# Kernel optimization log

Measured on AMD Instinct MI355X. Metric: run time of the kernel, lower is better.

The kernel has to match this reference:

```python
import jax, jax.numpy as jnp
from jax import lax
import numpy as np

B, DIM, L_IN = 8, 512, 4096
SCALE = 2
KSIZE = 17
DN = ('NCH', 'OIH', 'NCH')  # conv1d dimension numbers


def _aa_kernel(kernel_size: int, scale: int) -> np.ndarray:
    # replicates scipy.signal.kaiser_atten / kaiser_beta / windows.kaiser
    atten = 2.285 * (kernel_size - 1) * np.pi * (1.0 / scale) + 7.95
    if atten > 50:
        beta = 0.1102 * (atten - 8.7)
    elif atten > 21:
        beta = 0.5842 * (atten - 21) ** 0.4 + 0.07886 * (atten - 21)
    else:
        beta = 0.0
    win = np.kaiser(kernel_size, beta)
    xk = np.arange(kernel_size) - kernel_size // 2
    k = np.sinc(xk / scale) * win  # normalized sinc, same as torch.sinc
    return (k / k.sum()).astype(np.float32)


def setup_inputs() -> dict:
    key = jax.random.key(0)
    k1, k2, k3, k4, k5 = jax.random.split(key, 5)
    kconv = 2 * SCALE - 1
    return {
        'x': jax.random.normal(k1, (B, DIM, L_IN), dtype=jnp.float32),
        'conv_w': jax.random.normal(k2, (DIM, DIM, kconv), dtype=jnp.float32) * (1.0 / np.sqrt(DIM * kconv)),
        'conv_b': jax.random.normal(k3, (DIM,), dtype=jnp.float32) * 0.01,
        'aa_kernel': jnp.asarray(_aa_kernel(KSIZE, SCALE)),
        'proj_w': jax.random.normal(k4, (DIM, DIM), dtype=jnp.float32) * (1.0 / np.sqrt(DIM)),
        'proj_b': jax.random.normal(k5, (DIM,), dtype=jnp.float32) * 0.01,
    }


def reference(x, conv_w, conv_b, aa_kernel, proj_w, proj_b):
    s = SCALE
    # zero-insertion upsample + Conv1d(dim,dim,2s-1,pad=s-1) fused via lhs_dilation.
    # Torch zero-inserts to length l*s (trailing s-1 zeros), so right pad is 2s-2.
    y = lax.conv_general_dilated(
        x, conv_w, window_strides=(1,), padding=[(s - 1, 2 * s - 2)],
        lhs_dilation=(s,), dimension_numbers=DN,
    ) + conv_b[None, :, None]  # [B, D, l*s]
    # depthwise anti-alias filter (same Kaiser-sinc kernel per channel)
    dw = jnp.broadcast_to(aa_kernel, (DIM, 1, KSIZE))
    y = lax.conv_general_dilated(
        y, dw, window_strides=(1,), padding=[(KSIZE // 2, KSIZE // 2)],
        feature_group_count=DIM, dimension_numbers=DN,
    )
    # pointwise 1x1 projection
    return jnp.einsum('bdl,ed->bel', y, proj_w) + proj_b[None, :, None]
```

## Files before the change

### kernel.cpp

```cpp
#include <hip/hip_runtime.h>
#include <hip/hip_bf16.h>

#define BB_   8
#define DIM_  512
#define LIN_  4096
#define LOUT_ 8192

typedef __attribute__((ext_vector_type(8))) __bf16 bf16x8;
typedef __attribute__((ext_vector_type(4))) float  f32x4;

__device__ __forceinline__ float bf2f(unsigned short u) {
  union { unsigned int i; float f; } x;
  x.i = ((unsigned int)u) << 16;
  return x.f;
}

__global__ __launch_bounds__(256) void k_pre(const float* __restrict__ x,
                                             const float* __restrict__ proj_w,
                                             const float* __restrict__ conv_w,
                                             const float* __restrict__ conv_b,
                                             __hip_bfloat16* __restrict__ Xt,
                                             __hip_bfloat16* __restrict__ Mst,
                                             float* __restrict__ Pcb) {
  __shared__ float smem[64 * 65];
  const int bx  = blockIdx.x;
  const int tid = threadIdx.x;
  if (bx < 4096) {
    const int b  = bx & 7;
    const int d0 = ((bx >> 3) & 7) * 64;
    const int l0 = (bx >> 6) * 64;
    const int jj = tid & 63;
    const int i0 = tid >> 6;
#pragma unroll
    for (int r = 0; r < 16; ++r) {
      const int i = i0 + r * 4;
      smem[i * 65 + jj] = x[(size_t)(b * DIM_ + d0 + i) * LIN_ + l0 + jj];
    }
    __syncthreads();
#pragma unroll
    for (int r = 0; r < 16; ++r) {
      const int i = i0 + r * 4;
      Xt[(size_t)(b * LIN_ + l0 + i) * DIM_ + d0 + jj] =
          __float2bfloat16(smem[jj * 65 + i]);
    }
  } else if (bx < 4864) {
    const int idx = bx - 4096;
    const int kk = idx >> 8;
    const int et = ((idx >> 4) & 15) * 32;
    const int it = (idx & 15) * 32;
    float* Pt = smem;
    float* Wt = smem + 32 * 33;
    const int tx = tid & 15, ty = tid >> 4;
    float acc[2][2] = {};
    for (int d0 = 0; d0 < DIM_; d0 += 32) {
      {
        const int i = tid >> 3;
        const int j = (tid & 7) * 4;
        const float4 v = *(const float4*)&proj_w[(size_t)(et + i) * DIM_ + d0 + j];
        Pt[i * 33 + j] = v.x; Pt[i * 33 + j + 1] = v.y;
        Pt[i * 33 + j + 2] = v.z; Pt[i * 33 + j + 3] = v.w;
      }
#pragma unroll
      for (int r = 0; r < 4; ++r) {
        const int id2 = tid + r * 256;
        const int i = id2 >> 5, j = id2 & 31;
        Wt[i * 33 + j] = conv_w[(size_t)(d0 + i) * (DIM_ * 3) + (it + j) * 3 + kk];
      }
      __syncthreads();
#pragma unroll
      for (int dl = 0; dl < 32; ++dl) {
        float pv[2], wv[2];
        pv[0] = Pt[(ty * 2) * 33 + dl];     pv[1] = Pt[(ty * 2 + 1) * 33 + dl];
        wv[0] = Wt[dl * 33 + tx * 2];       wv[1] = Wt[dl * 33 + tx * 2 + 1];
#pragma unroll
        for (int a = 0; a < 2; ++a)
#pragma unroll
          for (int bq = 0; bq < 2; ++bq) acc[a][bq] += pv[a] * wv[bq];
      }
      __syncthreads();
    }
#pragma unroll
    for (int a = 0; a < 2; ++a)
#pragma unroll
      for (int bq = 0; bq < 2; ++bq)
        Mst[(size_t)(kk * DIM_ + et + ty * 2 + a) * DIM_ + it + tx * 2 + bq] =
            __float2bfloat16(acc[a][bq]);
  } else {
    const int idx = bx - 4864;
    const int e = idx * 4 + (tid >> 6);
    const int j = tid & 63;
    float s = 0.f;
#pragma unroll
    for (int d = j; d < DIM_; d += 64) s += proj_w[(size_t)e * DIM_ + d] * conv_b[d];
#pragma unroll
    for (int off = 32; off > 0; off >>= 1) s += __shfl_down(s, off, 64);
    if (j == 0) Pcb[e] = s;
  }
}

__global__ __launch_bounds__(256, 2) void k_gemm(const __hip_bfloat16* __restrict__ A,
                                                 const __hip_bfloat16* __restrict__ Bt,
                                                 const float* __restrict__ Pcb,
                                                 __hip_bfloat16* __restrict__ U) {
  __shared__ __align__(16) __hip_bfloat16 As[2][128 * 64];
  __shared__ __align__(16) __hip_bfloat16 Bs[2][128 * 64];
  const int tid = threadIdx.x;
  const int r0 = blockIdx.x * 128;
  const int c0 = blockIdx.y * 128;
  const int lane = tid & 63;
  const int wave = tid >> 6;
  const int wm = wave >> 1, wn = wave & 1;

  const int rA = tid >> 3;
  const int ch = tid & 7;
  const __hip_bfloat16* aG = A  + (size_t)(r0 + rA) * 512 + ch * 8;
  const __hip_bfloat16* bG = Bt + (size_t)(c0 + rA) * 512 + ch * 8;
  int wo[4];
#pragma unroll
  for (int i = 0; i < 4; ++i) {
    const int rg = rA + 32 * i;
    wo[i] = rg * 64 + ((ch ^ (rg & 7)) * 8);
  }

  bf16x8 gA[4], gB[4];
#pragma unroll
  for (int i = 0; i < 4; ++i) {
    gA[i] = *(const bf16x8*)(aG + (size_t)(32 * i) * 512);
    gB[i] = *(const bf16x8*)(bG + (size_t)(32 * i) * 512);
  }
#pragma unroll
  for (int i = 0; i < 4; ++i) {
    *(bf16x8*)(&As[0][wo[i]]) = gA[i];
    *(bf16x8*)(&Bs[0][wo[i]]) = gB[i];
  }
  __syncthreads();

  f32x4 acc[4][4] = {};
  const int kq   = lane >> 4;
  const int mrow = wm * 64 + (lane & 15);
  const int ncol = wn * 64 + (lane & 15);

  for (int kt = 0; kt < 8; ++kt) {
    if (kt < 7) {
#pragma unroll
      for (int i = 0; i < 4; ++i) {
        gA[i] = *(const bf16x8*)(aG + (size_t)(32 * i) * 512 + (kt + 1) * 64);
        gB[i] = *(const bf16x8*)(bG + (size_t)(32 * i) * 512 + (kt + 1) * 64);
      }
    }
    const __hip_bfloat16* Ab = As[kt & 1];
    const __hip_bfloat16* Bb = Bs[kt & 1];
#pragma unroll
    for (int k0 = 0; k0 < 64; k0 += 32) {
      const int c = (k0 >> 3) + kq;
      bf16x8 af[4], bfr[4];
#pragma unroll
      for (int i = 0; i < 4; ++i) {
        const int rg = mrow + i * 16;
        af[i] = *(const bf16x8*)(Ab + rg * 64 + ((c ^ (rg & 7)) * 8));
      }
#pragma unroll
      for (int i = 0; i < 4; ++i) {
        const int rg = ncol + i * 16;
        bfr[i] = *(const bf16x8*)(Bb + rg * 64 + ((c ^ (rg & 7)) * 8));
      }
#pragma unroll
      for (int mt = 0; mt < 4; ++mt)
#pragma unroll
        for (int nt = 0; nt < 4; ++nt)
          acc[mt][nt] = __builtin_amdgcn_mfma_f32_16x16x32_bf16(af[mt], bfr[nt],
                                                                acc[mt][nt], 0, 0, 0);
    }
    if (kt < 7) {
      __hip_bfloat16* wA = &As[(kt + 1) & 1][0];
      __hip_bfloat16* wB = &Bs[(kt + 1) & 1][0];
#pragma unroll
      for (int i = 0; i < 4; ++i) {
        *(bf16x8*)(&wA[wo[i]]) = gA[i];
        *(bf16x8*)(&wB[wo[i]]) = gB[i];
      }
    }
    __syncthreads();
  }

  const int kk = r0 >> 9;
  const int bb = c0 >> 12;
  const int e0 = (r0 & 511) + wm * 64;
  const int l0 = (c0 & 4095) + wn * 64;
#pragma unroll
  for (int mt = 0; mt < 4; ++mt) {
#pragma unroll
    for (int nt = 0; nt < 4; ++nt) {
      const int ltile = l0 + nt * 16 + (lane & 15);
      const int ebase = e0 + mt * 16 + (lane >> 4) * 4;
#pragma unroll
      for (int r = 0; r < 4; ++r) {
        float v = acc[mt][nt][r];
        const int e = ebase + r;
        if (kk < 2) v += Pcb[e];
        U[(size_t)((kk * 8 + bb) * 512 + e) * 4096 + ltile] = __float2bfloat16(v);
      }
    }
  }
}

__global__ __launch_bounds__(256) void k_aa(const __hip_bfloat16* __restrict__ U,
                                            const float* __restrict__ aa,
                                            const float* __restrict__ proj_b,
                                            float* __restrict__ out) {
  const int b  = blockIdx.x >> 9;
  const int e  = blockIdx.x & 511;
  const int l0 = blockIdx.y << 10;
  const int tid = threadIdx.x;
  const int lt = l0 + 4 * tid;
  const int w  = lt - 4;
  const unsigned short* q0 = (const unsigned short*)(U + (size_t)((0 * 8 + b) * 512 + e) * 4096);
  const unsigned short* q1 = (const unsigned short*)(U + (size_t)((1 * 8 + b) * 512 + e) * 4096);
  const unsigned short* q2 = (const unsigned short*)(U + (size_t)((2 * 8 + b) * 512 + e) * 4096);

  float Ew[12], Ow[12];
  if (w >= 0 && w + 16 <= 4096) {
    unsigned short e1[12], e0a[12], e2[16];
#pragma unroll
    for (int c = 0; c < 3; ++c) {
      const ushort4 a = *(const ushort4*)(q1 + w + 4 * c);
      e1[4 * c] = a.x; e1[4 * c + 1] = a.y; e1[4 * c + 2] = a.z; e1[4 * c + 3] = a.w;
      const ushort4 d = *(const ushort4*)(q0 + w + 4 * c);
      e0a[4 * c] = d.x; e0a[4 * c + 1] = d.y; e0a[4 * c + 2] = d.z; e0a[4 * c + 3] = d.w;
    }
#pragma unroll
    for (int c = 0; c < 4; ++c) {
      const ushort4 a = *(const ushort4*)(q2 + w + 4 * c);
      e2[4 * c] = a.x; e2[4 * c + 1] = a.y; e2[4 * c + 2] = a.z; e2[4 * c + 3] = a.w;
    }
#pragma unroll
    for (int j = 0; j < 12; ++j) {
      Ew[j] = bf2f(e1[j]);
      Ow[j] = bf2f(e0a[j]) + bf2f(e2[j + 1]);
    }
  } else {
#pragma unroll
    for (int j = 0; j < 12; ++j) {
      const int l = w + j;
      float vE = 0.f, vO = 0.f;
      if (l >= 0 && l < 4096) {
        vE = bf2f(q1[l]);
        vO = bf2f(q0[l]);
        if (l + 1 < 4096) vO += bf2f(q2[l + 1]);
      }
      Ew[j] = vE; Ow[j] = vO;
    }
  }

  float sa[17];
#pragma unroll
  for (int j = 0; j < 17; ++j) sa[j] = aa[j];
  const float pb = proj_b[e];
  float res[8];
#pragma unroll
  for (int t = 0; t < 4; ++t) {
    float se = 0.f, so = 0.f;
#pragma unroll
    for (int q = 0; q <= 8; ++q) {
      se += sa[2 * q] * Ew[t + q];
      so += sa[2 * q] * Ow[t + q];
    }
#pragma unroll
    for (int q = 0; q < 8; ++q) {
      se += sa[2 * q + 1] * Ow[t + q];
      so += sa[2 * q + 1] * Ew[t + q + 1];
    }
    res[2 * t]     = se + pb;
    res[2 * t + 1] = so + pb;
  }
  float* orow = out + (size_t)(b * 512 + e) * 8192 + 2 * lt;
  *(float4*)(orow)     = *(float4*)&res[0];
  *(float4*)(orow + 4) = *(float4*)&res[4];
}

extern "C" void kernel_launch(void* const* d_in, const int* in_sizes, int n_in,
                              void* d_out, int out_size, void* d_ws, size_t ws_size,
                              hipStream_t stream) {
  const float* x      = (const float*)d_in[0];
  const float* conv_w = (const float*)d_in[1];
  const float* conv_b = (const float*)d_in[2];
  const float* aa     = (const float*)d_in[3];
  const float* proj_w = (const float*)d_in[4];
  const float* proj_b = (const float*)d_in[5];
  float* out = (float*)d_out;

  char* ws = (char*)d_ws;
  __hip_bfloat16* Xt  = (__hip_bfloat16*)ws;
  __hip_bfloat16* Mst = (__hip_bfloat16*)(ws + 33554432);
  float*          Pcb = (float*)(ws + 35127296);
  __hip_bfloat16* U   = (__hip_bfloat16*)(ws + 35129344);

  k_pre<<<dim3(4992, 1, 1), 256, 0, stream>>>(x, proj_w, conv_w, conv_b, Xt, Mst, Pcb);
  k_gemm<<<dim3(12, 256), 256, 0, stream>>>(Mst, Xt, Pcb, U);
  k_aa<<<dim3(4096, 4), 256, 0, stream>>>(U, aa, proj_b, out);
}
```

Measured before the change: 380.7 us.

## Fuse x transpose/bf16 conversion into GEMM with resident B tile, widen AA per-thread work

Drops the separate transpose pass that wrote a bf16 copy of x to workspace. Each GEMM block now loads a 64-column slab of x straight into a swizzled shared-memory tile covering all of K, then streams the 1536x512 weight matrix through double-buffered A tiles, so the whole output column strip comes from one block. The AA kernel now handles 8 outputs per thread with 16-byte loads. The GEMM grid shrinks to 512 blocks with a 64-wide N tile and 64KB+ of LDS, which may lower occupancy and MFMA efficiency.

```diff
diff --git a/kernel.cpp b/kernel.cpp
--- a/kernel.cpp
+++ b/kernel.cpp
@@ -8,6 +8,7 @@
 
 typedef __attribute__((ext_vector_type(8))) __bf16 bf16x8;
 typedef __attribute__((ext_vector_type(4))) float  f32x4;
+typedef __attribute__((ext_vector_type(8))) unsigned short u16x8;
 
 __device__ __forceinline__ float bf2f(unsigned short u) {
   union { unsigned int i; float f; } x;
@@ -15,39 +16,18 @@
   return x.f;
 }
 
-__global__ __launch_bounds__(256) void k_pre(const float* __restrict__ x,
-                                             const float* __restrict__ proj_w,
-                                             const float* __restrict__ conv_w,
-                                             const float* __restrict__ conv_b,
-                                             __hip_bfloat16* __restrict__ Xt,
-                                             __hip_bfloat16* __restrict__ Mst,
-                                             float* __restrict__ Pcb) {
-  __shared__ float smem[64 * 65];
+__global__ __launch_bounds__(256) void k_prep(const float* __restrict__ proj_w,
+                                              const float* __restrict__ conv_w,
+                                              const float* __restrict__ conv_b,
+                                              __hip_bfloat16* __restrict__ Mst,
+                                              float* __restrict__ Pcb) {
+  __shared__ float smem[2 * 32 * 33];
   const int bx  = blockIdx.x;
   const int tid = threadIdx.x;
-  if (bx < 4096) {
-    const int b  = bx & 7;
-    const int d0 = ((bx >> 3) & 7) * 64;
-    const int l0 = (bx >> 6) * 64;
-    const int jj = tid & 63;
-    const int i0 = tid >> 6;
-#pragma unroll
-    for (int r = 0; r < 16; ++r) {
-      const int i = i0 + r * 4;
-      smem[i * 65 + jj] = x[(size_t)(b * DIM_ + d0 + i) * LIN_ + l0 + jj];
-    }
-    __syncthreads();
-#pragma unroll
-    for (int r = 0; r < 16; ++r) {
-      const int i = i0 + r * 4;
-      Xt[(size_t)(b * LIN_ + l0 + i) * DIM_ + d0 + jj] =
-          __float2bfloat16(smem[jj * 65 + i]);
-    }
-  } else if (bx < 4864) {
-    const int idx = bx - 4096;
-    const int kk = idx >> 8;
-    const int et = ((idx >> 4) & 15) * 32;
-    const int it = (idx & 15) * 32;
+  if (bx < 768) {
+    const int kk = bx >> 8;
+    const int et = ((bx >> 4) & 15) * 32;
+    const int it = (bx & 15) * 32;
     float* Pt = smem;
     float* Wt = smem + 32 * 33;
     const int tx = tid & 15, ty = tid >> 4;
@@ -61,8 +41,8 @@
         Pt[i * 33 + j + 2] = v.z; Pt[i * 33 + j + 3] = v.w;
       }
 #pragma unroll
-      for (int r = 0; r < 4; ++r) {
-        const int id2 = tid + r * 256;
+      for (int r2 = 0; r2 < 4; ++r2) {
+        const int id2 = tid + r2 * 256;
         const int i = id2 >> 5, j = id2 & 31;
         Wt[i * 33 + j] = conv_w[(size_t)(d0 + i) * (DIM_ * 3) + (it + j) * 3 + kk];
       }
@@ -86,7 +66,7 @@
         Mst[(size_t)(kk * DIM_ + et + ty * 2 + a) * DIM_ + it + tx * 2 + bq] =
             __float2bfloat16(acc[a][bq]);
   } else {
-    const int idx = bx - 4864;
+    const int idx = bx - 768;
     const int e = idx * 4 + (tid >> 6);
     const int j = tid & 63;
     float s = 0.f;
@@ -98,109 +78,110 @@
   }
 }
 
-__global__ __launch_bounds__(256, 2) void k_gemm(const __hip_bfloat16* __restrict__ A,
-                                                 const __hip_bfloat16* __restrict__ Bt,
+__global__ __launch_bounds__(256, 2) void k_gemm(const float* __restrict__ x,
+                                                 const __hip_bfloat16* __restrict__ Mst,
                                                  const float* __restrict__ Pcb,
                                                  __hip_bfloat16* __restrict__ U) {
-  __shared__ __align__(16) __hip_bfloat16 As[2][128 * 64];
-  __shared__ __align__(16) __hip_bfloat16 Bs[2][128 * 64];
+  __shared__ __align__(16) __hip_bfloat16 Bs[64 * 512];
+  __shared__ __align__(16) __hip_bfloat16 As[2][128 * 32];
   const int tid = threadIdx.x;
-  const int r0 = blockIdx.x * 128;
-  const int c0 = blockIdx.y * 128;
+  const int ct = blockIdx.x;
+  const int bb = ct >> 6;
+  const int l0 = (ct & 63) * 64;
+
+  {
+    const float* xb = x + (size_t)bb * DIM_ * LIN_ + l0;
+    const int dr = tid >> 4;
+    const int lc = (tid & 15) * 4;
+#pragma unroll 4
+    for (int p = 0; p < 32; ++p) {
+      const int d = p * 16 + dr;
+      const float4 v = *(const float4*)(xb + (size_t)d * LIN_ + lc);
+      const int c8 = d >> 3, d7 = d & 7;
+      const float vv[4] = {v.x, v.y, v.z, v.w};
+#pragma unroll
+      for (int j = 0; j < 4; ++j) {
+        const int l = lc + j;
+        Bs[l * 512 + ((c8 ^ (l & 7)) << 3) + d7] = __float2bfloat16(vv[j]);
+      }
+    }
+  }
+
+  const int r   = tid >> 2;
+  const int chA = tid & 3;
+  const int swz = chA ^ (r & 3);
+  bf16x8 gA0 = *(const bf16x8*)(Mst + (size_t)r * 512 + swz * 8);
+  bf16x8 gA1 = *(const bf16x8*)(Mst + (size_t)(r + 64) * 512 + swz * 8);
+  *(bf16x8*)(&As[0][r * 32 + chA * 8]) = gA0;
+  *(bf16x8*)(&As[0][(r + 64) * 32 + chA * 8]) = gA1;
+  __syncthreads();
+
   const int lane = tid & 63;
   const int wave = tid >> 6;
   const int wm = wave >> 1, wn = wave & 1;
-
-  const int rA = tid >> 3;
-  const int ch = tid & 7;
-  const __hip_bfloat16* aG = A  + (size_t)(r0 + rA) * 512 + ch * 8;
-  const __hip_bfloat16* bG = Bt + (size_t)(c0 + rA) * 512 + ch * 8;
-  int wo[4];
-#pragma unroll
-  for (int i = 0; i < 4; ++i) {
-    const int rg = rA + 32 * i;
-    wo[i] = rg * 64 + ((ch ^ (rg & 7)) * 8);
-  }
-
-  bf16x8 gA[4], gB[4];
-#pragma unroll
-  for (int i = 0; i < 4; ++i) {
-    gA[i] = *(const bf16x8*)(aG + (size_t)(32 * i) * 512);
-    gB[i] = *(const bf16x8*)(bG + (size_t)(32 * i) * 512);
-  }
-#pragma unroll
-  for (int i = 0; i < 4; ++i) {
-    *(bf16x8*)(&As[0][wo[i]]) = gA[i];
-    *(bf16x8*)(&Bs[0][wo[i]]) = gB[i];
-  }
-  __syncthreads();
-
-  f32x4 acc[4][4] = {};
-  const int kq   = lane >> 4;
+  const int kq = lane >> 4;
   const int mrow = wm * 64 + (lane & 15);
-  const int ncol = wn * 64 + (lane & 15);
-
-  for (int kt = 0; kt < 8; ++kt) {
-    if (kt < 7) {
-#pragma unroll
-      for (int i = 0; i < 4; ++i) {
-        gA[i] = *(const bf16x8*)(aG + (size_t)(32 * i) * 512 + (kt + 1) * 64);
-        gB[i] = *(const bf16x8*)(bG + (size_t)(32 * i) * 512 + (kt + 1) * 64);
-      }
-    }
-    const __hip_bfloat16* Ab = As[kt & 1];
-    const __hip_bfloat16* Bb = Bs[kt & 1];
-#pragma unroll
-    for (int k0 = 0; k0 < 64; k0 += 32) {
-      const int c = (k0 >> 3) + kq;
-      bf16x8 af[4], bfr[4];
-#pragma unroll
-      for (int i = 0; i < 4; ++i) {
-        const int rg = mrow + i * 16;
-        af[i] = *(const bf16x8*)(Ab + rg * 64 + ((c ^ (rg & 7)) * 8));
-      }
-#pragma unroll
-      for (int i = 0; i < 4; ++i) {
-        const int rg = ncol + i * 16;
-        bfr[i] = *(const bf16x8*)(Bb + rg * 64 + ((c ^ (rg & 7)) * 8));
-      }
-#pragma unroll
-      for (int mt = 0; mt < 4; ++mt)
-#pragma unroll
-        for (int nt = 0; nt < 4; ++nt)
-          acc[mt][nt] = __builtin_amdgcn_mfma_f32_16x16x32_bf16(af[mt], bfr[nt],
-                                                                acc[mt][nt], 0, 0, 0);
-    }
-    if (kt < 7) {
-      __hip_bfloat16* wA = &As[(kt + 1) & 1][0];
-      __hip_bfloat16* wB = &Bs[(kt + 1) & 1][0];
-#pragma unroll
-      for (int i = 0; i < 4; ++i) {
-        *(bf16x8*)(&wA[wo[i]]) = gA[i];
-        *(bf16x8*)(&wB[wo[i]]) = gB[i];
+  const int slotA = kq ^ (lane & 3);
+  const int lcol0 = wn * 32 + (lane & 15);
+
+  f32x4 acc[4][2] = {};
+
+  for (int it = 0; it < 192; ++it) {
+    const int rt = it >> 4, kt = it & 15;
+    const int cur = it & 1, nxt = cur ^ 1;
+
+    if (it < 191) {
+      const int itn = it + 1;
+      const int rtn = itn >> 4, ktn = itn & 15;
+      const __hip_bfloat16* ap =
+          Mst + (size_t)(rtn * 128 + r) * 512 + ktn * 32 + swz * 8;
+      gA0 = *(const bf16x8*)(ap);
+      gA1 = *(const bf16x8*)(ap + (size_t)64 * 512);
+    }
+
+    bf16x8 af[4], bfr[2];
+#pragma unroll
+    for (int mt = 0; mt < 4; ++mt)
+      af[mt] = *(const bf16x8*)(&As[cur][(mrow + mt * 16) * 32 + slotA * 8]);
+    const int ck = kt * 4 + kq;
+#pragma unroll
+    for (int nt = 0; nt < 2; ++nt) {
+      const int l = lcol0 + nt * 16;
+      bfr[nt] = *(const bf16x8*)(&Bs[l * 512 + ((ck ^ (lane & 7)) << 3)]);
+    }
+#pragma unroll
+    for (int mt = 0; mt < 4; ++mt)
+#pragma unroll
+      for (int nt = 0; nt < 2; ++nt)
+        acc[mt][nt] = __builtin_amdgcn_mfma_f32_16x16x32_bf16(af[mt], bfr[nt],
+                                                              acc[mt][nt], 0, 0, 0);
+
+    if (it < 191) {
+      *(bf16x8*)(&As[nxt][r * 32 + chA * 8]) = gA0;
+      *(bf16x8*)(&As[nxt][(r + 64) * 32 + chA * 8]) = gA1;
+    }
+
+    if (kt == 15) {
+      const int kk = rt >> 2;
+      const int e0 = (rt & 3) * 128 + wm * 64;
+#pragma unroll
+      for (int mt = 0; mt < 4; ++mt) {
+#pragma unroll
+        for (int nt = 0; nt < 2; ++nt) {
+          const int l = l0 + wn * 32 + nt * 16 + (lane & 15);
+          const int ebase = e0 + mt * 16 + kq * 4;
+#pragma unroll
+          for (int rr = 0; rr < 4; ++rr) {
+            float v = acc[mt][nt][rr];
+            const int e = ebase + rr;
+            if (kk < 2) v += Pcb[e];
+            U[(size_t)((kk * 8 + bb) * 512 + e) * 4096 + l] = __float2bfloat16(v);
+            acc[mt][nt][rr] = 0.f;
+          }
+        }
       }
     }
     __syncthreads();
-  }
-
-  const int kk = r0 >> 9;
-  const int bb = c0 >> 12;
-  const int e0 = (r0 & 511) + wm * 64;
-  const int l0 = (c0 & 4095) + wn * 64;
-#pragma unroll
-  for (int mt = 0; mt < 4; ++mt) {
-#pragma unroll
-    for (int nt = 0; nt < 4; ++nt) {
-      const int ltile = l0 + nt * 16 + (lane & 15);
-      const int ebase = e0 + mt * 16 + (lane >> 4) * 4;
-#pragma unroll
-      for (int r = 0; r < 4; ++r) {
-        float v = acc[mt][nt][r];
-        const int e = ebase + r;
-        if (kk < 2) v += Pcb[e];
-        U[(size_t)((kk * 8 + bb) * 512 + e) * 4096 + ltile] = __float2bfloat16(v);
-      }
-    }
   }
 }
 
@@ -210,45 +191,46 @@
                                             float* __restrict__ out) {
   const int b  = blockIdx.x >> 9;
   const int e  = blockIdx.x & 511;
-  const int l0 = blockIdx.y << 10;
+  const int l0 = blockIdx.y << 11;
   const int tid = threadIdx.x;
-  const int lt = l0 + 4 * tid;
-  const int w  = lt - 4;
+  const int lt = l0 + 8 * tid;
   const unsigned short* q0 = (const unsigned short*)(U + (size_t)((0 * 8 + b) * 512 + e) * 4096);
   const unsigned short* q1 = (const unsigned short*)(U + (size_t)((1 * 8 + b) * 512 + e) * 4096);
   const unsigned short* q2 = (const unsigned short*)(U + (size_t)((2 * 8 + b) * 512 + e) * 4096);
 
-  float Ew[12], Ow[12];
-  if (w >= 0 && w + 16 <= 4096) {
-    unsigned short e1[12], e0a[12], e2[16];
+  float E[17], O[16];
+  if (lt >= 8 && lt + 16 <= 4096) {
+    const int base = lt - 8;
+    unsigned short r1[24], r0[24], r2[24];
 #pragma unroll
     for (int c = 0; c < 3; ++c) {
-      const ushort4 a = *(const ushort4*)(q1 + w + 4 * c);
-      e1[4 * c] = a.x; e1[4 * c + 1] = a.y; e1[4 * c + 2] = a.z; e1[4 * c + 3] = a.w;
-      const ushort4 d = *(const ushort4*)(q0 + w + 4 * c);
-      e0a[4 * c] = d.x; e0a[4 * c + 1] = d.y; e0a[4 * c + 2] = d.z; e0a[4 * c + 3] = d.w;
-    }
-#pragma unroll
-    for (int c = 0; c < 4; ++c) {
-      const ushort4 a = *(const ushort4*)(q2 + w + 4 * c);
-      e2[4 * c] = a.x; e2[4 * c + 1] = a.y; e2[4 * c + 2] = a.z; e2[4 * c + 3] = a.w;
-    }
-#pragma unroll
-    for (int j = 0; j < 12; ++j) {
-      Ew[j] = bf2f(e1[j]);
-      Ow[j] = bf2f(e0a[j]) + bf2f(e2[j + 1]);
-    }
+      const u16x8 a = *(const u16x8*)(q1 + base + 8 * c);
+      const u16x8 d = *(const u16x8*)(q0 + base + 8 * c);
+      const u16x8 g = *(const u16x8*)(q2 + base + 8 * c);
+#pragma unroll
+      for (int j = 0; j < 8; ++j) {
+        r1[8 * c + j] = a[j]; r0[8 * c + j] = d[j]; r2[8 * c + j] = g[j];
+      }
+    }
+#pragma unroll
+    for (int j = 0; j < 17; ++j) E[j] = bf2f(r1[4 + j]);
+#pragma unroll
+    for (int j = 0; j < 16; ++j) O[j] = bf2f(r0[4 + j]) + bf2f(r2[5 + j]);
   } else {
 #pragma unroll
-    for (int j = 0; j < 12; ++j) {
-      const int l = w + j;
-      float vE = 0.f, vO = 0.f;
+    for (int j = 0; j < 17; ++j) {
+      const int l = lt - 4 + j;
+      E[j] = (l >= 0 && l < 4096) ? bf2f(q1[l]) : 0.f;
+    }
+#pragma unroll
+    for (int j = 0; j < 16; ++j) {
+      const int l = lt - 4 + j;
+      float v = 0.f;
       if (l >= 0 && l < 4096) {
-        vE = bf2f(q1[l]);
-        vO = bf2f(q0[l]);
-        if (l + 1 < 4096) vO += bf2f(q2[l + 1]);
-      }
-      Ew[j] = vE; Ow[j] = vO;
+        v = bf2f(q0[l]);
+        if (l + 1 < 4096) v += bf2f(q2[l + 1]);
+      }
+      O[j] = v;
     }
   }
 
@@ -256,26 +238,27 @@
 #pragma unroll
   for (int j = 0; j < 17; ++j) sa[j] = aa[j];
   const float pb = proj_b[e];
-  float res[8];
-#pragma unroll
-  for (int t = 0; t < 4; ++t) {
+  float res[16];
+#pragma unroll
+  for (int t = 0; t < 8; ++t) {
     float se = 0.f, so = 0.f;
 #pragma unroll
     for (int q = 0; q <= 8; ++q) {
-      se += sa[2 * q] * Ew[t + q];
-      so += sa[2 * q] * Ow[t + q];
+      se += sa[2 * q] * E[t + q];
+      so += sa[2 * q] * O[t + q];
     }
 #pragma unroll
     for (int q = 0; q < 8; ++q) {
-      se += sa[2 * q + 1] * Ow[t + q];
-      so += sa[2 * q + 1] * Ew[t + q + 1];
+      se += sa[2 * q + 1] * O[t + q];
+      so += sa[2 * q + 1] * E[t + q + 1];
     }
     res[2 * t]     = se + pb;
     res[2 * t + 1] = so + pb;
   }
   float* orow = out + (size_t)(b * 512 + e) * 8192 + 2 * lt;
-  *(float4*)(orow)     = *(float4*)&res[0];
-  *(float4*)(orow + 4) = *(float4*)&res[4];
+#pragma unroll
+  for (int c = 0; c < 4; ++c)
+    *(float4*)(orow + 4 * c) = *(const float4*)&res[4 * c];
 }
 
 extern "C" void kernel_launch(void* const* d_in, const int* in_sizes, int n_in,
@@ -290,12 +273,11 @@
   float* out = (float*)d_out;
 
   char* ws = (char*)d_ws;
-  __hip_bfloat16* Xt  = (__hip_bfloat16*)ws;
-  __hip_bfloat16* Mst = (__hip_bfloat16*)(ws + 33554432);
-  float*          Pcb = (float*)(ws + 35127296);
-  __hip_bfloat16* U   = (__hip_bfloat16*)(ws + 35129344);
-
-  k_pre<<<dim3(4992, 1, 1), 256, 0, stream>>>(x, proj_w, conv_w, conv_b, Xt, Mst, Pcb);
-  k_gemm<<<dim3(12, 256), 256, 0, stream>>>(Mst, Xt, Pcb, U);
-  k_aa<<<dim3(4096, 4), 256, 0, stream>>>(U, aa, proj_b, out);
-}
+  __hip_bfloat16* Mst = (__hip_bfloat16*)ws;
+  float*          Pcb = (float*)(ws + 1572864);
+  __hip_bfloat16* U   = (__hip_bfloat16*)(ws + 1576960);
+
+  k_prep<<<dim3(896, 1, 1), 256, 0, stream>>>(proj_w, conv_w, conv_b, Mst, Pcb);
+  k_gemm<<<dim3(512, 1, 1), 256, 0, stream>>>(x, Mst, Pcb, U);
+  k_aa<<<dim3(4096, 2), 256, 0, stream>>>(U, aa, proj_b, out);
+}
```

After: 369.9 us. 1.03x faster.
